# Kernel optimization log

Hardware: AMD Instinct MI355X
Metric: run time of the kernel (lower is better)

The kernel has to match this reference:

```python
import jax, jax.numpy as jnp
import numpy as np

N_NODES = 50000
N_EDGES = 800000
IN_CH = 128
OUT_CH = 64
HID = 2 * OUT_CH  # 128
NEG_SLOPE = 0.2  # PyG GATConv default negative_slope


def gat_conv(x, edge_index, W, a_src, a_dst, b):
    """Single-head PyG GATConv (heads=1, concat=True, self-loops already in edge_index)."""
    N = x.shape[0]
    h = x @ W  # [N, C]
    src, dst = edge_index[0], edge_index[1]
    # per-edge attention logits: leaky_relu(a_src . h_src + a_dst . h_dst)
    e = jax.nn.leaky_relu((h @ a_src)[src] + (h @ a_dst)[dst], NEG_SLOPE)  # [E]
    # softmax over incoming edges of each dst node (numerically stable)
    m = jax.ops.segment_max(e, dst, num_segments=N)
    p = jnp.exp(e - m[dst])
    denom = jax.ops.segment_sum(p, dst, num_segments=N)
    coef = p / denom[dst]  # [E]
    # scatter-aggregate weighted source features
    out = jax.ops.segment_sum(coef[:, None] * h[src], dst, num_segments=N)  # [N, C]
    return out + b


def setup_inputs() -> dict:
    key = jax.random.key(0)
    ks = jax.random.split(key, 12)
    s_in = 1.0 / np.sqrt(IN_CH)
    s_h = 1.0 / np.sqrt(HID)
    return {
        "x": jax.random.normal(ks[0], (N_NODES, IN_CH), dtype=jnp.float32),
        "edge_index": jax.random.randint(ks[1], (2, N_EDGES), 0, N_NODES, dtype=jnp.int64),
        "W1": jax.random.normal(ks[2], (IN_CH, HID), dtype=jnp.float32) * s_in,
        "a_src1": jax.random.normal(ks[3], (HID,), dtype=jnp.float32) * s_h,
        "a_dst1": jax.random.normal(ks[4], (HID,), dtype=jnp.float32) * s_h,
        "b1": jnp.zeros((HID,), dtype=jnp.float32),
        "W_mu": jax.random.normal(ks[5], (HID, OUT_CH), dtype=jnp.float32) * s_h,
        "a_src_mu": jax.random.normal(ks[6], (OUT_CH,), dtype=jnp.float32) * 0.125,
        "a_dst_mu": jax.random.normal(ks[7], (OUT_CH,), dtype=jnp.float32) * 0.125,
        "b_mu": jnp.zeros((OUT_CH,), dtype=jnp.float32),
        "W_ls": jax.random.normal(ks[8], (HID, OUT_CH), dtype=jnp.float32) * s_h,
        "a_src_ls": jax.random.normal(ks[9], (OUT_CH,), dtype=jnp.float32) * 0.125,
        "a_dst_ls": jax.random.normal(ks[10], (OUT_CH,), dtype=jnp.float32) * 0.125,
        "b_ls": jnp.zeros((OUT_CH,), dtype=jnp.float32),
    }


def reference(x, edge_index, W1, a_src1, a_dst1, b1, W_mu, a_src_mu, a_dst_mu, b_mu, W_ls, a_src_ls, a_dst_ls, b_ls):
    N = x.shape[0]
    loops = jnp.arange(N, dtype=edge_index.dtype)
    ei = jnp.concatenate([edge_index, jnp.stack([loops, loops])], axis=1)  # add self-loops
    h = jax.nn.relu(gat_conv(x, ei, W1, a_src1, a_dst1, b1))
    mu = gat_conv(h, ei, W_mu, a_src_mu, a_dst_mu, b_mu)
    logstd = gat_conv(h, ei, W_ls, a_src_ls, a_dst_ls, b_ls)
    return mu, logstd
```

## Files before the change

### kernel.cpp

```cpp
#include <hip/hip_runtime.h>
#include <hip/hip_bf16.h>
#include <math.h>

typedef __attribute__((ext_vector_type(8))) _Float16 half8;
typedef __attribute__((ext_vector_type(4))) float f32x4;


__device__ __forceinline__ float leaky02(float v) { return v > 0.0f ? v : 0.2f * v; }

__device__ __forceinline__ unsigned short f2bf(float f) {
  unsigned u = __float_as_uint(f);
  u += 0x7FFF + ((u >> 16) & 1);
  return (unsigned short)(u >> 16);
}
__device__ __forceinline__ float2 bfp(unsigned v) {
  float2 r;
  r.x = __uint_as_float(v << 16);
  r.y = __uint_as_float(v & 0xFFFF0000u);
  return r;
}


#define BSHIFT 8
#define BDSTS 256

__global__ __launch_bounds__(256) void bucket_scan_kernel(
    const int* __restrict__ bcount, int* __restrict__ bstart, int* __restrict__ bcursor,
    int* __restrict__ row_start, int NBUCK, int E, int N) {
  __shared__ int lds[256];
  int t = threadIdx.x;
  int v = (t < NBUCK) ? bcount[t] : 0;
  lds[t] = v;
  __syncthreads();
#pragma unroll
  for (int off = 1; off < 256; off <<= 1) {
    int tmp = (t >= off) ? lds[t - off] : 0;
    __syncthreads();
    lds[t] += tmp;
    __syncthreads();
  }
  if (t < NBUCK) {
    int excl = lds[t] - v;
    bstart[t] = excl;
    bcursor[t] = excl;
  }
  if (t == 0) { bstart[NBUCK] = E; row_start[N] = E; }
}

#define CHUNK 4096
__global__ __launch_bounds__(256) void pair_scatter_kernel(
    const int* __restrict__ ei, int* __restrict__ bcursor, unsigned* __restrict__ pairs, int E) {
  __shared__ int h[256], base[256], cur[256];
  h[threadIdx.x] = 0; cur[threadIdx.x] = 0;
  __syncthreads();
  int c0 = blockIdx.x * CHUNK;
  int c1 = min(c0 + CHUNK, E);
  for (int e = c0 + (int)threadIdx.x; e < c1; e += 256)
    atomicAdd(&h[ei[E + e] >> BSHIFT], 1);
  __syncthreads();
  if (h[threadIdx.x])
    base[threadIdx.x] = atomicAdd(&bcursor[threadIdx.x], h[threadIdx.x]);
  __syncthreads();
  for (int e = c0 + (int)threadIdx.x; e < c1; e += 256) {
    int dst = ei[E + e];
    int src = ei[e];
    int b = dst >> BSHIFT;
    int r = atomicAdd(&cur[b], 1);
    pairs[base[b] + r] = ((unsigned)src << BSHIFT) | (unsigned)(dst & (BDSTS - 1));
  }
}

__global__ __launch_bounds__(256) void fine_kernel(
    const unsigned* __restrict__ pairs, const int* __restrict__ bstart,
    int* __restrict__ row_start, int* __restrict__ esrc, int N) {
  __shared__ int h[BDSTS], sc[BDSTS], cur[BDSTS];
  int t = threadIdx.x;
  int b = blockIdx.x;
  int d0 = b << BSHIFT;
  int beg = bstart[b], end = bstart[b + 1];
  h[t] = 0;
  __syncthreads();
  for (int i = beg + t; i < end; i += 256) atomicAdd(&h[pairs[i] & (BDSTS - 1)], 1);
  __syncthreads();
  int v = h[t];
  sc[t] = v;
  __syncthreads();
#pragma unroll
  for (int off = 1; off < BDSTS; off <<= 1) {
    int tmp = (t >= off) ? sc[t - off] : 0;
    __syncthreads();
    sc[t] += tmp;
    __syncthreads();
  }
  int excl = sc[t] - v;
  if (d0 + t < N) row_start[d0 + t] = beg + excl;
  cur[t] = excl;
  __syncthreads();
  for (int i = beg + t; i < end; i += 256) {
    unsigned p = pairs[i];
    int r = atomicAdd(&cur[p & (BDSTS - 1)], 1);
    esrc[beg + r] = (int)(p >> BSHIFT);
  }
}


__global__ __launch_bounds__(256) void prep_w_kernel(
    const float* __restrict__ W1, const float* __restrict__ Wmu, const float* __restrict__ Wls,
    _Float16* __restrict__ Wt1, _Float16* __restrict__ Wt2) {
  int idx = blockIdx.x * 256 + threadIdx.x;
  int c = idx >> 7, k = idx & 127;
  Wt1[idx] = (_Float16)W1[k * 128 + c];
  float w2 = (c < 64) ? Wmu[k * 64 + c] : Wls[k * 64 + (c - 64)];
  Wt2[idx] = (_Float16)w2;
}


__global__ __launch_bounds__(256) void gemm1_hist(
    const float* __restrict__ X, const _Float16* __restrict__ Wt,
    const float* __restrict__ a_src, const float* __restrict__ a_dst,
    unsigned short* __restrict__ Hb, float* __restrict__ asrc, float* __restrict__ adst, int N,
    const int* __restrict__ ei, int* __restrict__ bcount, int E, int nGB) {
  if ((int)blockIdx.x >= nGB) {
    __shared__ int h[256];
    h[threadIdx.x] = 0;
    __syncthreads();
    int hb = (int)blockIdx.x - nGB;
    int c0 = hb * 2048;
    int c1 = min(c0 + 2048, E);
    for (int e = c0 + (int)threadIdx.x; e < c1; e += 256)
      atomicAdd(&h[ei[E + e] >> BSHIFT], 1);
    __syncthreads();
    if (h[threadIdx.x]) atomicAdd(&bcount[threadIdx.x], h[threadIdx.x]);
    return;
  }
  const int wid = threadIdx.x >> 6, lane = threadIdx.x & 63;
  const int r16 = ((int)blockIdx.x * 4 + wid) * 16;
  if (r16 >= N) return;
  const int cg = lane & 15;
  const int kq = (lane >> 4) * 8;
  const int rA = r16 + cg;
  const int rowClamp = min(rA, N - 1);

  f32x4 acc[8];
#pragma unroll
  for (int j = 0; j < 8; ++j) acc[j] = (f32x4){0.f, 0.f, 0.f, 0.f};

#pragma unroll
  for (int ks = 0; ks < 4; ++ks) {
    const int k0 = ks * 32;
    const float* xp = X + (size_t)rowClamp * 128 + k0 + kq;
    float4 xa = *(const float4*)xp;
    float4 xb = *(const float4*)(xp + 4);
    half8 a;
    a[0] = (_Float16)xa.x; a[1] = (_Float16)xa.y; a[2] = (_Float16)xa.z; a[3] = (_Float16)xa.w;
    a[4] = (_Float16)xb.x; a[5] = (_Float16)xb.y; a[6] = (_Float16)xb.z; a[7] = (_Float16)xb.w;
#pragma unroll
    for (int j = 0; j < 8; ++j) {
      half8 b = *(const half8*)(Wt + (size_t)(16 * j + cg) * 128 + k0 + kq);
      acc[j] = __builtin_amdgcn_mfma_f32_16x16x32_f16(a, b, acc[j], 0, 0, 0);
    }
  }

  float as_[8], ds_[8];
#pragma unroll
  for (int j = 0; j < 8; ++j) { as_[j] = a_src[16 * j + cg]; ds_[j] = a_dst[16 * j + cg]; }
  const int rg = (lane >> 4) * 4;
#pragma unroll
  for (int reg = 0; reg < 4; ++reg) {
    int row = r16 + rg + reg;
    bool ok = row < N;
    float ps = 0.f, pd = 0.f;
#pragma unroll
    for (int j = 0; j < 8; ++j) {
      float v = acc[j][reg];
      if (ok) Hb[(size_t)row * 128 + 16 * j + cg] = f2bf(v);
      ps = fmaf(v, as_[j], ps);
      pd = fmaf(v, ds_[j], pd);
    }
#pragma unroll
    for (int o = 1; o < 16; o <<= 1) { ps += __shfl_xor(ps, o); pd += __shfl_xor(pd, o); }
    if (ok && cg == 0) { asrc[row] = ps; adst[row] = pd; }
  }
}

__global__ __launch_bounds__(256) void gemm2_mfma(
    const _Float16* __restrict__ Xh, const _Float16* __restrict__ Wt,
    const float* __restrict__ a_src_mu, const float* __restrict__ a_dst_mu,
    const float* __restrict__ a_src_ls, const float* __restrict__ a_dst_ls,
    unsigned short* __restrict__ Hb, float* __restrict__ as2, float* __restrict__ ad2, int N) {
  const int wid = threadIdx.x >> 6, lane = threadIdx.x & 63;
  const int r16 = ((int)blockIdx.x * 4 + wid) * 16;
  if (r16 >= N) return;
  const int cg = lane & 15;
  const int kq = (lane >> 4) * 8;
  const int rA = r16 + cg;
  const int rowClamp = min(rA, N - 1);

  f32x4 acc[8];
#pragma unroll
  for (int j = 0; j < 8; ++j) acc[j] = (f32x4){0.f, 0.f, 0.f, 0.f};

#pragma unroll
  for (int ks = 0; ks < 4; ++ks) {
    const int k0 = ks * 32;
    half8 a = *(const half8*)(Xh + (size_t)rowClamp * 128 + k0 + kq);
#pragma unroll
    for (int j = 0; j < 8; ++j) {
      half8 b = *(const half8*)(Wt + (size_t)(16 * j + cg) * 128 + k0 + kq);
      acc[j] = __builtin_amdgcn_mfma_f32_16x16x32_f16(a, b, acc[j], 0, 0, 0);
    }
  }

  float asv[8], adv[8];
#pragma unroll
  for (int j = 0; j < 4; ++j) {
    asv[j] = a_src_mu[16 * j + cg]; adv[j] = a_dst_mu[16 * j + cg];
    asv[j + 4] = a_src_ls[16 * j + cg]; adv[j + 4] = a_dst_ls[16 * j + cg];
  }
  const int rg = (lane >> 4) * 4;
#pragma unroll
  for (int reg = 0; reg < 4; ++reg) {
    int row = r16 + rg + reg;
    bool ok = row < N;
    float psm = 0.f, pdm = 0.f, psl = 0.f, pdl = 0.f;
#pragma unroll
    for (int j = 0; j < 8; ++j) {
      float v = acc[j][reg];
      if (ok) Hb[(size_t)row * 128 + 16 * j + cg] = f2bf(v);
      if (j < 4) { psm = fmaf(v, asv[j], psm); pdm = fmaf(v, adv[j], pdm); }
      else       { psl = fmaf(v, asv[j], psl); pdl = fmaf(v, adv[j], pdl); }
    }
#pragma unroll
    for (int o = 1; o < 16; o <<= 1) {
      psm += __shfl_xor(psm, o); pdm += __shfl_xor(pdm, o);
      psl += __shfl_xor(psl, o); pdl += __shfl_xor(pdl, o);
    }
    if (ok && cg == 0) {
      as2[2 * row] = psm; ad2[2 * row] = pdm;
      as2[2 * row + 1] = psl; ad2[2 * row + 1] = pdl;
    }
  }
}


#define GATH(K)                                                          \
  {                                                                      \
    int sA = __shfl(s, hbase + jj + K);                                  \
    float wA = __shfl(w, hbase + jj + K);                                \
    uint2 hA = *(const uint2*)(Hb + (size_t)sA * 128 + sub * 4);         \
    float2 pa = bfp(hA.x), pb = bfp(hA.y);                               \
    a0 = fmaf(wA, pa.x, a0); a1 = fmaf(wA, pa.y, a1);                    \
    a2 = fmaf(wA, pb.x, a2); a3 = fmaf(wA, pb.y, a3);                    \
  }

__global__ __launch_bounds__(256) void agg1_ns(
    const unsigned short* __restrict__ Hb, const float* __restrict__ asrc,
    const float* __restrict__ adst, const int* __restrict__ row_start,
    const int* __restrict__ esrc, const float* __restrict__ b,
    _Float16* __restrict__ hout, int N) {
  const int lane = threadIdx.x & 63;
  const int half = lane >> 5, sub = lane & 31;
  const int g = (int)(blockIdx.x * 4 + (threadIdx.x >> 6));
  const int d = g * 2 + half;
  const bool dok = d < N;
  const int dc = dok ? d : N - 1;
  const float ad = adst[dc];
  const float wself = __expf(leaky02(asrc[dc] + ad));
  uint2 sv = *(const uint2*)(Hb + (size_t)dc * 128 + sub * 4);
  float2 f0 = bfp(sv.x), f1 = bfp(sv.y);
  float a0 = wself * f0.x, a1 = wself * f0.y, a2 = wself * f1.x, a3 = wself * f1.y;
  float den = (sub == 0) ? wself : 0.f;
  const int beg = row_start[dc];
  const int n = dok ? (row_start[dc + 1] - beg) : 0;
  const int nmax = max(n, __shfl_xor(n, 32));
  const int hbase = half * 32;
  for (int c0 = 0; c0 < nmax; c0 += 32) {
    int j = c0 + sub;
    bool v = j < n;
    int s = v ? esrc[beg + j] : 0;
    float w = 0.f;
    if (v) w = __expf(leaky02(asrc[s] + ad));
    den += w;
    int cnt = n - c0;
    if (cnt > 32) cnt = 32;
    if (cnt < 0) cnt = 0;
    int jj = 0;
    for (; jj + 8 <= cnt; jj += 8) {
      GATH(0) GATH(1) GATH(2) GATH(3) GATH(4) GATH(5) GATH(6) GATH(7)
    }
    for (; jj < cnt; ++jj) GATH(0)
  }
#pragma unroll
  for (int o = 16; o > 0; o >>= 1) den += __shfl_xor(den, o);
  if (dok) {
    float inv = 1.0f / den;
    float4 bv = *(const float4*)(b + sub * 4);
    _Float16 o4[4];
    o4[0] = (_Float16)fmaxf(fmaf(a0, inv, bv.x), 0.f);
    o4[1] = (_Float16)fmaxf(fmaf(a1, inv, bv.y), 0.f);
    o4[2] = (_Float16)fmaxf(fmaf(a2, inv, bv.z), 0.f);
    o4[3] = (_Float16)fmaxf(fmaf(a3, inv, bv.w), 0.f);
    *(uint2*)(hout + (size_t)d * 128 + sub * 4) = *(uint2*)o4;
  }
}


#define GATH2(K)                                                         \
  {                                                                      \
    int sA = __shfl(s, hbase + jj + K);                                  \
    float wmA = __shfl(wm, hbase + jj + K);                              \
    float wlA = __shfl(wl, hbase + jj + K);                              \
    float wA = isMu ? wmA : wlA;                                         \
    uint2 hA = *(const uint2*)(Hb + (size_t)sA * 128 + sub * 4);         \
    float2 pa = bfp(hA.x), pb = bfp(hA.y);                               \
    a0 = fmaf(wA, pa.x, a0); a1 = fmaf(wA, pa.y, a1);                    \
    a2 = fmaf(wA, pb.x, a2); a3 = fmaf(wA, pb.y, a3);                    \
  }

__global__ __launch_bounds__(256) void agg2_ns(
    const unsigned short* __restrict__ Hb,
    const float2* __restrict__ as2, const float2* __restrict__ ad2,
    const int* __restrict__ row_start, const int* __restrict__ esrc,
    const float* __restrict__ b_mu, const float* __restrict__ b_ls,
    float* __restrict__ out_mu, float* __restrict__ out_ls, int N) {
  const int lane = threadIdx.x & 63;
  const int half = lane >> 5, sub = lane & 31;
  const bool isMu = sub < 16;
  const int g = (int)(blockIdx.x * 4 + (threadIdx.x >> 6));
  const int d = g * 2 + half;
  const bool dok = d < N;
  const int dc = dok ? d : N - 1;
  const float2 adv = ad2[dc];
  const float2 asv = as2[dc];
  const float wself_m = __expf(leaky02(asv.x + adv.x));
  const float wself_l = __expf(leaky02(asv.y + adv.y));
  uint2 sv = *(const uint2*)(Hb + (size_t)dc * 128 + sub * 4);
  float2 f0 = bfp(sv.x), f1 = bfp(sv.y);
  const float wself = isMu ? wself_m : wself_l;
  float a0 = wself * f0.x, a1 = wself * f0.y, a2 = wself * f1.x, a3 = wself * f1.y;
  float den_m = (sub == 0) ? wself_m : 0.f;
  float den_l = (sub == 0) ? wself_l : 0.f;
  const int beg = row_start[dc];
  const int n = dok ? (row_start[dc + 1] - beg) : 0;
  const int nmax = max(n, __shfl_xor(n, 32));
  const int hbase = half * 32;
  for (int c0 = 0; c0 < nmax; c0 += 32) {
    int j = c0 + sub;
    bool v = j < n;
    int s = v ? esrc[beg + j] : 0;
    float wm = 0.f, wl = 0.f;
    if (v) {
      float2 av = as2[s];
      wm = __expf(leaky02(av.x + adv.x));
      wl = __expf(leaky02(av.y + adv.y));
    }
    den_m += wm;
    den_l += wl;
    int cnt = n - c0;
    if (cnt > 32) cnt = 32;
    if (cnt < 0) cnt = 0;
    int jj = 0;
    for (; jj + 8 <= cnt; jj += 8) {
      GATH2(0) GATH2(1) GATH2(2) GATH2(3) GATH2(4) GATH2(5) GATH2(6) GATH2(7)
    }
    for (; jj < cnt; ++jj) GATH2(0)
  }
#pragma unroll
  for (int o = 16; o > 0; o >>= 1) {
    den_m += __shfl_xor(den_m, o);
    den_l += __shfl_xor(den_l, o);
  }
  if (dok) {
    float inv = isMu ? (1.0f / den_m) : (1.0f / den_l);
    const float* bp;
    float* op;
    if (isMu) { bp = b_mu + sub * 4; op = out_mu + (size_t)d * 64 + sub * 4; }
    else      { bp = b_ls + sub * 4 - 64; op = out_ls + (size_t)d * 64 + sub * 4 - 64; }
    float4 bv = *(const float4*)bp;
    float4 o;
    o.x = fmaf(a0, inv, bv.x);
    o.y = fmaf(a1, inv, bv.y);
    o.z = fmaf(a2, inv, bv.z);
    o.w = fmaf(a3, inv, bv.w);
    *(float4*)op = o;
  }
}


extern "C" void kernel_launch(void* const* d_in, const int* in_sizes, int n_in,
                              void* d_out, int out_size, void* d_ws, size_t ws_size,
                              hipStream_t stream) {
  const float* x = (const float*)d_in[0];
  const int* ei = (const int*)d_in[1];
  const float* W1 = (const float*)d_in[2];
  const float* a_src1 = (const float*)d_in[3];
  const float* a_dst1 = (const float*)d_in[4];
  const float* b1 = (const float*)d_in[5];
  const float* W_mu = (const float*)d_in[6];
  const float* a_src_mu = (const float*)d_in[7];
  const float* a_dst_mu = (const float*)d_in[8];
  const float* b_mu = (const float*)d_in[9];
  const float* W_ls = (const float*)d_in[10];
  const float* a_src_ls = (const float*)d_in[11];
  const float* a_dst_ls = (const float*)d_in[12];
  const float* b_ls = (const float*)d_in[13];

  const int N = in_sizes[0] / 128;
  const int E = in_sizes[1] / 2;
  const int NBUCK = (N + BDSTS - 1) >> BSHIFT;

  uint8_t* p = (uint8_t*)d_ws;
  auto carve = [&](size_t bytes) -> void* {
    void* q = (void*)p;
    p += (bytes + 255) & ~(size_t)255;
    return q;
  };
  int* bcount = (int*)carve((size_t)(NBUCK + 1) * 4);
  int* bstart = (int*)carve((size_t)(NBUCK + 1) * 4);
  int* bcursor = (int*)carve((size_t)NBUCK * 4);
  int* row_start = (int*)carve((size_t)(N + 1) * 4);
  int* esrc = (int*)carve((size_t)E * 4);
  unsigned* pairs = (unsigned*)carve((size_t)E * 4);
  unsigned short* Hb1 = (unsigned short*)carve((size_t)N * 128 * 2);
  _Float16* h1 = (_Float16*)carve((size_t)N * 128 * 2);
  _Float16* Wt1 = (_Float16*)carve((size_t)128 * 128 * 2);
  _Float16* Wt2 = (_Float16*)carve((size_t)128 * 128 * 2);
  float* as1 = (float*)carve((size_t)N * 4);
  float* ad1 = (float*)carve((size_t)N * 4);
  float* as2 = (float*)carve((size_t)N * 8);
  float* ad2 = (float*)carve((size_t)N * 8);

  unsigned short* Hb2 = Hb1;

  hipMemsetAsync(bcount, 0, (size_t)(NBUCK + 1) * 4, stream);
  prep_w_kernel<<<64, 256, 0, stream>>>(W1, W_mu, W_ls, Wt1, Wt2);

  const int nGB = (N + 63) / 64;
  const int nHB = (E + 2047) / 2048;
  gemm1_hist<<<nGB + nHB, 256, 0, stream>>>(x, Wt1, a_src1, a_dst1, Hb1, as1, ad1, N,
                                            ei, bcount, E, nGB);
  bucket_scan_kernel<<<1, 256, 0, stream>>>(bcount, bstart, bcursor, row_start, NBUCK, E, N);
  pair_scatter_kernel<<<(E + CHUNK - 1) / CHUNK, 256, 0, stream>>>(ei, bcursor, pairs, E);
  fine_kernel<<<NBUCK, 256, 0, stream>>>(pairs, bstart, row_start, esrc, N);

  const int nwaves = (N + 1) / 2;
  const int nblk = (nwaves + 3) / 4;
  agg1_ns<<<nblk, 256, 0, stream>>>(Hb1, as1, ad1, row_start, esrc, b1, h1, N);
  gemm2_mfma<<<(N + 63) / 64, 256, 0, stream>>>(h1, Wt2, a_src_mu, a_dst_mu,
                                                a_src_ls, a_dst_ls, Hb2, as2, ad2, N);
  float* out_mu = (float*)d_out;
  float* out_ls = out_mu + (size_t)N * 64;
  agg2_ns<<<nblk, 256, 0, stream>>>(Hb2, (const float2*)as2, (const float2*)ad2,
                                    row_start, esrc, b_mu, b_ls, out_mu, out_ls, N);
}
```

Measured before the change: 163.4 us.

## Widen aggregation gathers to 16-byte loads and fold bucket scan into histogram kernel

The aggregation kernels now have each half-wave split into two 16-lane groups. Each group loads 8 bf16 features per lane with a 16-byte load and handles alternate edges, and the two partial sums are combined with a shuffle at the end, so fewer, wider gather instructions are issued. The separate bucket-scan kernel and the memset are removed: prep_w zeroes the counters, and the last histogram block, detected with an atomic done counter, performs the prefix scan. This saves two launches but relies on a threadfence/atomic last-block pattern and adds shuffle reductions in the aggregation kernels.

```diff
diff --git a/kernel.cpp b/kernel.cpp
--- a/kernel.cpp
+++ b/kernel.cpp
@@ -23,29 +23,6 @@
 
 #define BSHIFT 8
 #define BDSTS 256
-
-__global__ __launch_bounds__(256) void bucket_scan_kernel(
-    const int* __restrict__ bcount, int* __restrict__ bstart, int* __restrict__ bcursor,
-    int* __restrict__ row_start, int NBUCK, int E, int N) {
-  __shared__ int lds[256];
-  int t = threadIdx.x;
-  int v = (t < NBUCK) ? bcount[t] : 0;
-  lds[t] = v;
-  __syncthreads();
-#pragma unroll
-  for (int off = 1; off < 256; off <<= 1) {
-    int tmp = (t >= off) ? lds[t - off] : 0;
-    __syncthreads();
-    lds[t] += tmp;
-    __syncthreads();
-  }
-  if (t < NBUCK) {
-    int excl = lds[t] - v;
-    bstart[t] = excl;
-    bcursor[t] = excl;
-  }
-  if (t == 0) { bstart[NBUCK] = E; row_start[N] = E; }
-}
 
 #define CHUNK 4096
 __global__ __launch_bounds__(256) void pair_scatter_kernel(
@@ -106,12 +83,17 @@
 
 __global__ __launch_bounds__(256) void prep_w_kernel(
     const float* __restrict__ W1, const float* __restrict__ Wmu, const float* __restrict__ Wls,
-    _Float16* __restrict__ Wt1, _Float16* __restrict__ Wt2) {
+    _Float16* __restrict__ Wt1, _Float16* __restrict__ Wt2,
+    int* __restrict__ bcount, int* __restrict__ done, int NBUCK) {
   int idx = blockIdx.x * 256 + threadIdx.x;
   int c = idx >> 7, k = idx & 127;
   Wt1[idx] = (_Float16)W1[k * 128 + c];
   float w2 = (c < 64) ? Wmu[k * 64 + c] : Wls[k * 64 + (c - 64)];
   Wt2[idx] = (_Float16)w2;
+  if (blockIdx.x == 0) {
+    if ((int)threadIdx.x <= NBUCK) bcount[threadIdx.x] = 0;
+    if (threadIdx.x == 255) *done = 0;
+  }
 }
 
 
@@ -119,9 +101,12 @@
     const float* __restrict__ X, const _Float16* __restrict__ Wt,
     const float* __restrict__ a_src, const float* __restrict__ a_dst,
     unsigned short* __restrict__ Hb, float* __restrict__ asrc, float* __restrict__ adst, int N,
-    const int* __restrict__ ei, int* __restrict__ bcount, int E, int nGB) {
+    const int* __restrict__ ei, int* __restrict__ bcount, int E, int nGB, int nHB,
+    int* __restrict__ bstart, int* __restrict__ bcursor, int* __restrict__ row_start,
+    int* __restrict__ done, int NBUCK) {
   if ((int)blockIdx.x >= nGB) {
     __shared__ int h[256];
+    __shared__ int lastFlag;
     h[threadIdx.x] = 0;
     __syncthreads();
     int hb = (int)blockIdx.x - nGB;
@@ -131,6 +116,31 @@
       atomicAdd(&h[ei[E + e] >> BSHIFT], 1);
     __syncthreads();
     if (h[threadIdx.x]) atomicAdd(&bcount[threadIdx.x], h[threadIdx.x]);
+    __syncthreads();
+    if (threadIdx.x == 0) {
+      __threadfence();
+      lastFlag = (atomicAdd(done, 1) == nHB - 1) ? 1 : 0;
+    }
+    __syncthreads();
+    if (lastFlag) {
+      int t = threadIdx.x;
+      int v = (t < NBUCK) ? atomicAdd(&bcount[t], 0) : 0;
+      h[t] = v;
+      __syncthreads();
+#pragma unroll
+      for (int off = 1; off < 256; off <<= 1) {
+        int tmp = (t >= off) ? h[t - off] : 0;
+        __syncthreads();
+        h[t] += tmp;
+        __syncthreads();
+      }
+      if (t < NBUCK) {
+        int excl = h[t] - v;
+        bstart[t] = excl;
+        bcursor[t] = excl;
+      }
+      if (t == 0) { bstart[NBUCK] = E; row_start[N] = E; }
+    }
     return;
   }
   const int wid = threadIdx.x >> 6, lane = threadIdx.x & 63;
@@ -138,8 +148,7 @@
   if (r16 >= N) return;
   const int cg = lane & 15;
   const int kq = (lane >> 4) * 8;
-  const int rA = r16 + cg;
-  const int rowClamp = min(rA, N - 1);
+  const int rowClamp = min(r16 + cg, N - 1);
 
   f32x4 acc[8];
 #pragma unroll
@@ -193,8 +202,7 @@
   if (r16 >= N) return;
   const int cg = lane & 15;
   const int kq = (lane >> 4) * 8;
-  const int rA = r16 + cg;
-  const int rowClamp = min(rA, N - 1);
+  const int rowClamp = min(r16 + cg, N - 1);
 
   f32x4 acc[8];
 #pragma unroll
@@ -243,32 +251,40 @@
 }
 
 
-#define GATH(K)                                                          \
-  {                                                                      \
-    int sA = __shfl(s, hbase + jj + K);                                  \
-    float wA = __shfl(w, hbase + jj + K);                                \
-    uint2 hA = *(const uint2*)(Hb + (size_t)sA * 128 + sub * 4);         \
-    float2 pa = bfp(hA.x), pb = bfp(hA.y);                               \
-    a0 = fmaf(wA, pa.x, a0); a1 = fmaf(wA, pa.y, a1);                    \
-    a2 = fmaf(wA, pb.x, a2); a3 = fmaf(wA, pb.y, a3);                    \
-  }
-
-__global__ __launch_bounds__(256) void agg1_ns(
+#define STEP1(J)                                                          \
+  {                                                                       \
+    int idx = (J) + grp;                                                  \
+    int sA = __shfl(s, hbase + idx);                                      \
+    float wA = __shfl(w, hbase + idx);                                    \
+    uint4 hv = *(const uint4*)(Hb + (size_t)sA * 128 + li * 8);           \
+    float2 q0 = bfp(hv.x), q1 = bfp(hv.y), q2 = bfp(hv.z), q3 = bfp(hv.w);\
+    a0 = fmaf(wA, q0.x, a0); a1 = fmaf(wA, q0.y, a1);                     \
+    a2 = fmaf(wA, q1.x, a2); a3 = fmaf(wA, q1.y, a3);                     \
+    a4 = fmaf(wA, q2.x, a4); a5 = fmaf(wA, q2.y, a5);                     \
+    a6 = fmaf(wA, q3.x, a6); a7 = fmaf(wA, q3.y, a7);                     \
+  }
+
+__global__ __launch_bounds__(256) void agg1_g16(
     const unsigned short* __restrict__ Hb, const float* __restrict__ asrc,
     const float* __restrict__ adst, const int* __restrict__ row_start,
     const int* __restrict__ esrc, const float* __restrict__ b,
     _Float16* __restrict__ hout, int N) {
   const int lane = threadIdx.x & 63;
   const int half = lane >> 5, sub = lane & 31;
+  const int grp = (lane >> 4) & 1, li = lane & 15;
   const int g = (int)(blockIdx.x * 4 + (threadIdx.x >> 6));
   const int d = g * 2 + half;
   const bool dok = d < N;
   const int dc = dok ? d : N - 1;
   const float ad = adst[dc];
   const float wself = __expf(leaky02(asrc[dc] + ad));
-  uint2 sv = *(const uint2*)(Hb + (size_t)dc * 128 + sub * 4);
-  float2 f0 = bfp(sv.x), f1 = bfp(sv.y);
-  float a0 = wself * f0.x, a1 = wself * f0.y, a2 = wself * f1.x, a3 = wself * f1.y;
+  float a0 = 0.f, a1 = 0.f, a2 = 0.f, a3 = 0.f, a4 = 0.f, a5 = 0.f, a6 = 0.f, a7 = 0.f;
+  if (grp == 0) {
+    uint4 sv = *(const uint4*)(Hb + (size_t)dc * 128 + li * 8);
+    float2 q0 = bfp(sv.x), q1 = bfp(sv.y), q2 = bfp(sv.z), q3 = bfp(sv.w);
+    a0 = wself * q0.x; a1 = wself * q0.y; a2 = wself * q1.x; a3 = wself * q1.y;
+    a4 = wself * q2.x; a5 = wself * q2.y; a6 = wself * q3.x; a7 = wself * q3.y;
+  }
   float den = (sub == 0) ? wself : 0.f;
   const int beg = row_start[dc];
   const int n = dok ? (row_start[dc + 1] - beg) : 0;
@@ -278,46 +294,66 @@
     int j = c0 + sub;
     bool v = j < n;
     int s = v ? esrc[beg + j] : 0;
-    float w = 0.f;
-    if (v) w = __expf(leaky02(asrc[s] + ad));
+    float w = v ? __expf(leaky02(asrc[s] + ad)) : 0.f;
     den += w;
     int cnt = n - c0;
-    if (cnt > 32) cnt = 32;
-    if (cnt < 0) cnt = 0;
+    cnt = min(max(cnt, 0), 32);
     int jj = 0;
-    for (; jj + 8 <= cnt; jj += 8) {
-      GATH(0) GATH(1) GATH(2) GATH(3) GATH(4) GATH(5) GATH(6) GATH(7)
-    }
-    for (; jj < cnt; ++jj) GATH(0)
-  }
+    for (; jj + 8 <= cnt; jj += 8) { STEP1(jj) STEP1(jj + 2) STEP1(jj + 4) STEP1(jj + 6) }
+    for (; jj < cnt; jj += 2) {
+      int idx = jj + grp;
+      int sA = __shfl(s, hbase + idx);
+      float wA = __shfl(w, hbase + idx);
+      if (idx < cnt) {
+        uint4 hv = *(const uint4*)(Hb + (size_t)sA * 128 + li * 8);
+        float2 q0 = bfp(hv.x), q1 = bfp(hv.y), q2 = bfp(hv.z), q3 = bfp(hv.w);
+        a0 = fmaf(wA, q0.x, a0); a1 = fmaf(wA, q0.y, a1);
+        a2 = fmaf(wA, q1.x, a2); a3 = fmaf(wA, q1.y, a3);
+        a4 = fmaf(wA, q2.x, a4); a5 = fmaf(wA, q2.y, a5);
+        a6 = fmaf(wA, q3.x, a6); a7 = fmaf(wA, q3.y, a7);
+      }
+    }
+  }
+  a0 += __shfl_xor(a0, 16); a1 += __shfl_xor(a1, 16);
+  a2 += __shfl_xor(a2, 16); a3 += __shfl_xor(a3, 16);
+  a4 += __shfl_xor(a4, 16); a5 += __shfl_xor(a5, 16);
+  a6 += __shfl_xor(a6, 16); a7 += __shfl_xor(a7, 16);
 #pragma unroll
   for (int o = 16; o > 0; o >>= 1) den += __shfl_xor(den, o);
-  if (dok) {
+  if (dok && grp == 0) {
     float inv = 1.0f / den;
-    float4 bv = *(const float4*)(b + sub * 4);
-    _Float16 o4[4];
-    o4[0] = (_Float16)fmaxf(fmaf(a0, inv, bv.x), 0.f);
-    o4[1] = (_Float16)fmaxf(fmaf(a1, inv, bv.y), 0.f);
-    o4[2] = (_Float16)fmaxf(fmaf(a2, inv, bv.z), 0.f);
-    o4[3] = (_Float16)fmaxf(fmaf(a3, inv, bv.w), 0.f);
-    *(uint2*)(hout + (size_t)d * 128 + sub * 4) = *(uint2*)o4;
-  }
-}
-
-
-#define GATH2(K)                                                         \
-  {                                                                      \
-    int sA = __shfl(s, hbase + jj + K);                                  \
-    float wmA = __shfl(wm, hbase + jj + K);                              \
-    float wlA = __shfl(wl, hbase + jj + K);                              \
-    float wA = isMu ? wmA : wlA;                                         \
-    uint2 hA = *(const uint2*)(Hb + (size_t)sA * 128 + sub * 4);         \
-    float2 pa = bfp(hA.x), pb = bfp(hA.y);                               \
-    a0 = fmaf(wA, pa.x, a0); a1 = fmaf(wA, pa.y, a1);                    \
-    a2 = fmaf(wA, pb.x, a2); a3 = fmaf(wA, pb.y, a3);                    \
-  }
-
-__global__ __launch_bounds__(256) void agg2_ns(
+    float4 b0 = *(const float4*)(b + li * 8);
+    float4 b1 = *(const float4*)(b + li * 8 + 4);
+    _Float16 o8[8];
+    o8[0] = (_Float16)fmaxf(fmaf(a0, inv, b0.x), 0.f);
+    o8[1] = (_Float16)fmaxf(fmaf(a1, inv, b0.y), 0.f);
+    o8[2] = (_Float16)fmaxf(fmaf(a2, inv, b0.z), 0.f);
+    o8[3] = (_Float16)fmaxf(fmaf(a3, inv, b0.w), 0.f);
+    o8[4] = (_Float16)fmaxf(fmaf(a4, inv, b1.x), 0.f);
+    o8[5] = (_Float16)fmaxf(fmaf(a5, inv, b1.y), 0.f);
+    o8[6] = (_Float16)fmaxf(fmaf(a6, inv, b1.z), 0.f);
+    o8[7] = (_Float16)fmaxf(fmaf(a7, inv, b1.w), 0.f);
+    *(uint4*)(hout + (size_t)d * 128 + li * 8) = *(uint4*)o8;
+  }
+}
+
+
+#define STEP2(J)                                                          \
+  {                                                                       \
+    int idx = (J) + grp;                                                  \
+    int sA = __shfl(s, hbase + idx);                                      \
+    float wmA = __shfl(wm, hbase + idx);                                  \
+    float wlA = __shfl(wl, hbase + idx);                                  \
+    float wA = isMu ? wmA : wlA;                                          \
+    uint4 hv = *(const uint4*)(Hb + (size_t)sA * 128 + li * 8);           \
+    float2 q0 = bfp(hv.x), q1 = bfp(hv.y), q2 = bfp(hv.z), q3 = bfp(hv.w);\
+    a0 = fmaf(wA, q0.x, a0); a1 = fmaf(wA, q0.y, a1);                     \
+    a2 = fmaf(wA, q1.x, a2); a3 = fmaf(wA, q1.y, a3);                     \
+    a4 = fmaf(wA, q2.x, a4); a5 = fmaf(wA, q2.y, a5);                     \
+    a6 = fmaf(wA, q3.x, a6); a7 = fmaf(wA, q3.y, a7);                     \
+  }
+
+__global__ __launch_bounds__(256) void agg2_g16(
     const unsigned short* __restrict__ Hb,
     const float2* __restrict__ as2, const float2* __restrict__ ad2,
     const int* __restrict__ row_start, const int* __restrict__ esrc,
@@ -325,7 +361,8 @@
     float* __restrict__ out_mu, float* __restrict__ out_ls, int N) {
   const int lane = threadIdx.x & 63;
   const int half = lane >> 5, sub = lane & 31;
-  const bool isMu = sub < 16;
+  const int grp = (lane >> 4) & 1, li = lane & 15;
+  const bool isMu = li < 8;
   const int g = (int)(blockIdx.x * 4 + (threadIdx.x >> 6));
   const int d = g * 2 + half;
   const bool dok = d < N;
@@ -334,10 +371,14 @@
   const float2 asv = as2[dc];
   const float wself_m = __expf(leaky02(asv.x + adv.x));
   const float wself_l = __expf(leaky02(asv.y + adv.y));
-  uint2 sv = *(const uint2*)(Hb + (size_t)dc * 128 + sub * 4);
-  float2 f0 = bfp(sv.x), f1 = bfp(sv.y);
-  const float wself = isMu ? wself_m : wself_l;
-  float a0 = wself * f0.x, a1 = wself * f0.y, a2 = wself * f1.x, a3 = wself * f1.y;
+  float a0 = 0.f, a1 = 0.f, a2 = 0.f, a3 = 0.f, a4 = 0.f, a5 = 0.f, a6 = 0.f, a7 = 0.f;
+  if (grp == 0) {
+    const float wself = isMu ? wself_m : wself_l;
+    uint4 sv = *(const uint4*)(Hb + (size_t)dc * 128 + li * 8);
+    float2 q0 = bfp(sv.x), q1 = bfp(sv.y), q2 = bfp(sv.z), q3 = bfp(sv.w);
+    a0 = wself * q0.x; a1 = wself * q0.y; a2 = wself * q1.x; a3 = wself * q1.y;
+    a4 = wself * q2.x; a5 = wself * q2.y; a6 = wself * q3.x; a7 = wself * q3.y;
+  }
   float den_m = (sub == 0) ? wself_m : 0.f;
   float den_l = (sub == 0) ? wself_l : 0.f;
   const int beg = row_start[dc];
@@ -357,32 +398,49 @@
     den_m += wm;
     den_l += wl;
     int cnt = n - c0;
-    if (cnt > 32) cnt = 32;
-    if (cnt < 0) cnt = 0;
+    cnt = min(max(cnt, 0), 32);
     int jj = 0;
-    for (; jj + 8 <= cnt; jj += 8) {
-      GATH2(0) GATH2(1) GATH2(2) GATH2(3) GATH2(4) GATH2(5) GATH2(6) GATH2(7)
-    }
-    for (; jj < cnt; ++jj) GATH2(0)
-  }
+    for (; jj + 8 <= cnt; jj += 8) { STEP2(jj) STEP2(jj + 2) STEP2(jj + 4) STEP2(jj + 6) }
+    for (; jj < cnt; jj += 2) {
+      int idx = jj + grp;
+      int sA = __shfl(s, hbase + idx);
+      float wmA = __shfl(wm, hbase + idx);
+      float wlA = __shfl(wl, hbase + idx);
+      float wA = isMu ? wmA : wlA;
+      if (idx < cnt) {
+        uint4 hv = *(const uint4*)(Hb + (size_t)sA * 128 + li * 8);
+        float2 q0 = bfp(hv.x), q1 = bfp(hv.y), q2 = bfp(hv.z), q3 = bfp(hv.w);
+        a0 = fmaf(wA, q0.x, a0); a1 = fmaf(wA, q0.y, a1);
+        a2 = fmaf(wA, q1.x, a2); a3 = fmaf(wA, q1.y, a3);
+        a4 = fmaf(wA, q2.x, a4); a5 = fmaf(wA, q2.y, a5);
+        a6 = fmaf(wA, q3.x, a6); a7 = fmaf(wA, q3.y, a7);
+      }
+    }
+  }
+  a0 += __shfl_xor(a0, 16); a1 += __shfl_xor(a1, 16);
+  a2 += __shfl_xor(a2, 16); a3 += __shfl_xor(a3, 16);
+  a4 += __shfl_xor(a4, 16); a5 += __shfl_xor(a5, 16);
+  a6 += __shfl_xor(a6, 16); a7 += __shfl_xor(a7, 16);
 #pragma unroll
   for (int o = 16; o > 0; o >>= 1) {
     den_m += __shfl_xor(den_m, o);
     den_l += __shfl_xor(den_l, o);
   }
-  if (dok) {
+  if (dok && grp == 0) {
     float inv = isMu ? (1.0f / den_m) : (1.0f / den_l);
     const float* bp;
     float* op;
-    if (isMu) { bp = b_mu + sub * 4; op = out_mu + (size_t)d * 64 + sub * 4; }
-    else      { bp = b_ls + sub * 4 - 64; op = out_ls + (size_t)d * 64 + sub * 4 - 64; }
-    float4 bv = *(const float4*)bp;
-    float4 o;
-    o.x = fmaf(a0, inv, bv.x);
-    o.y = fmaf(a1, inv, bv.y);
-    o.z = fmaf(a2, inv, bv.z);
-    o.w = fmaf(a3, inv, bv.w);
-    *(float4*)op = o;
+    if (isMu) { bp = b_mu + li * 8; op = out_mu + (size_t)d * 64 + li * 8; }
+    else      { bp = b_ls + (li - 8) * 8; op = out_ls + (size_t)d * 64 + (li - 8) * 8; }
+    float4 b0 = *(const float4*)bp;
+    float4 b1 = *(const float4*)(bp + 4);
+    float4 o0, o1;
+    o0.x = fmaf(a0, inv, b0.x); o0.y = fmaf(a1, inv, b0.y);
+    o0.z = fmaf(a2, inv, b0.z); o0.w = fmaf(a3, inv, b0.w);
+    o1.x = fmaf(a4, inv, b1.x); o1.y = fmaf(a5, inv, b1.y);
+    o1.z = fmaf(a6, inv, b1.z); o1.w = fmaf(a7, inv, b1.w);
+    *(float4*)op = o0;
+    *(float4*)(op + 4) = o1;
   }
 }
 
@@ -418,6 +476,7 @@
   int* bcount = (int*)carve((size_t)(NBUCK + 1) * 4);
   int* bstart = (int*)carve((size_t)(NBUCK + 1) * 4);
   int* bcursor = (int*)carve((size_t)NBUCK * 4);
+  int* done = (int*)carve(4);
   int* row_start = (int*)carve((size_t)(N + 1) * 4);
   int* esrc = (int*)carve((size_t)E * 4);
   unsigned* pairs = (unsigned*)carve((size_t)E * 4);
@@ -432,24 +491,23 @@
 
   unsigned short* Hb2 = Hb1;
 
-  hipMemsetAsync(bcount, 0, (size_t)(NBUCK + 1) * 4, stream);
-  prep_w_kernel<<<64, 256, 0, stream>>>(W1, W_mu, W_ls, Wt1, Wt2);
+  prep_w_kernel<<<64, 256, 0, stream>>>(W1, W_mu, W_ls, Wt1, Wt2, bcount, done, NBUCK);
 
   const int nGB = (N + 63) / 64;
   const int nHB = (E + 2047) / 2048;
   gemm1_hist<<<nGB + nHB, 256, 0, stream>>>(x, Wt1, a_src1, a_dst1, Hb1, as1, ad1, N,
-                                            ei, bcount, E, nGB);
-  bucket_scan_kernel<<<1, 256, 0, stream>>>(bcount, bstart, bcursor, row_start, NBUCK, E, N);
+                                            ei, bcount, E, nGB, nHB,
+                                            bstart, bcursor, row_start, done, NBUCK);
   pair_scatter_kernel<<<(E + CHUNK - 1) / CHUNK, 256, 0, stream>>>(ei, bcursor, pairs, E);
   fine_kernel<<<NBUCK, 256, 0, stream>>>(pairs, bstart, row_start, esrc, N);
 
   const int nwaves = (N + 1) / 2;
   const int nblk = (nwaves + 3) / 4;
-  agg1_ns<<<nblk, 256, 0, stream>>>(Hb1, as1, ad1, row_start, esrc, b1, h1, N);
+  agg1_g16<<<nblk, 256, 0, stream>>>(Hb1, as1, ad1, row_start, esrc, b1, h1, N);
   gemm2_mfma<<<(N + 63) / 64, 256, 0, stream>>>(h1, Wt2, a_src_mu, a_dst_mu,
                                                 a_src_ls, a_dst_ls, Hb2, as2, ad2, N);
   float* out_mu = (float*)d_out;
   float* out_ls = out_mu + (size_t)N * 64;
-  agg2_ns<<<nblk, 256, 0, stream>>>(Hb2, (const float2*)as2, (const float2*)ad2,
-                                    row_start, esrc, b_mu, b_ls, out_mu, out_ls, N);
-}
+  agg2_g16<<<nblk, 256, 0, stream>>>(Hb2, (const float2*)as2, (const float2*)ad2,
+                                     row_start, esrc, b_mu, b_ls, out_mu, out_ls, N);
+}
```

Result: no change. 161.3 us (-1.3%).
